# Optimization experiments

Measured on AMD Instinct MI355X. Metric: run time of the kernel, lower is better.

Reference implementation:

```python
import jax, jax.numpy as jnp
import numpy as np


def setup_inputs() -> dict:
    key = jax.random.key(0)
    k1, k2, k3, k4 = jax.random.split(key, 4)
    B, S, D = 2, 2048, 1024
    return {
        "X": jax.random.normal(k1, (B, S, D), dtype=jnp.float32),
        "W_q": jax.random.normal(k2, (D, D), dtype=jnp.float32),
        "W_k": jax.random.normal(k3, (D, D), dtype=jnp.float32),
        "W_v": jax.random.normal(k4, (D, D), dtype=jnp.float32),
        "n_heads": 16,
    }


def reference(X, W_q, W_k, W_v, n_heads):
    B, S, D = X.shape
    H = n_heads
    dh = D // H
    # QKV projections, split heads: [B,S,D] -> [H,B,S,dh]
    def split_heads(Y):
        return Y.reshape(B, S, H, dh).transpose(2, 0, 1, 3)
    Q = split_heads(X @ W_q)
    K = split_heads(X @ W_k)
    V = split_heads(X @ W_v)
    scale = 1.0 / jnp.sqrt(jnp.asarray(dh, dtype=X.dtype))
    # [H,B,S,S] attention scores (naive, matches the original)
    scores = jax.nn.softmax(jnp.einsum("hbqd,hbkd->hbqk", Q, K) * scale, axis=-1)
    out = jnp.einsum("hbqk,hbkd->hbqd", scores, V)  # [H,B,S,dh]
    # torch.concat(out, 0) over leading H dim -> [H*B, S, dh]
    return out.reshape(H * B, S, dh)
```

## Files before the change

kernel.cpp:

```cpp
#include <hip/hip_runtime.h>

typedef unsigned short u16;
typedef unsigned int u32;
typedef __bf16 bf16x8 __attribute__((ext_vector_type(8)));
typedef float f32x4 __attribute__((ext_vector_type(4)));
typedef float f32x16 __attribute__((ext_vector_type(16)));

#define WT_HI_E  ((size_t)0)
#define WT_LO_E  ((size_t)3 << 20)
#define X_HI_E   ((size_t)6 << 20)
#define X_LO_E   ((size_t)10 << 20)
#define Q_HI_E   ((size_t)14 << 20)
#define Q_LO_E   ((size_t)18 << 20)
#define K_HI_E   ((size_t)22 << 20)
#define K_LO_E   ((size_t)26 << 20)
#define V_HI_E   ((size_t)30 << 20)

__device__ __forceinline__ u16 bf16_rne(float x) {
  u32 u = __float_as_uint(x);
  u32 r = (u + 0x7fffu + ((u >> 16) & 1u)) >> 16;
  return (u16)r;
}
__device__ __forceinline__ float bf16_f(u16 h) {
  return __uint_as_float(((u32)h) << 16);
}

__device__ __forceinline__ void gload16(const u16* g, u16* l) {
  __builtin_amdgcn_global_load_lds(
      (const __attribute__((address_space(1))) void*)g,
      (__attribute__((address_space(3))) void*)l, 16, 0, 0);
}

__global__ __launch_bounds__(256) void k_xsplit(const float* __restrict__ X,
                                                u16* __restrict__ ws) {
  u16* xh = ws + X_HI_E;
  u16* xl = ws + X_LO_E;
  size_t i = ((size_t)blockIdx.x * 256 + threadIdx.x) * 8;
  float4 a = *(const float4*)(X + i);
  float4 b = *(const float4*)(X + i + 4);
  float v[8] = {a.x, a.y, a.z, a.w, b.x, b.y, b.z, b.w};
  u32 Hh[4], Ll[4];
#pragma unroll
  for (int j = 0; j < 4; j++) {
    u16 h0 = bf16_rne(v[2 * j]);
    u16 l0 = bf16_rne(v[2 * j] - bf16_f(h0));
    u16 h1 = bf16_rne(v[2 * j + 1]);
    u16 l1 = bf16_rne(v[2 * j + 1] - bf16_f(h1));
    Hh[j] = (u32)h0 | ((u32)h1 << 16);
    Ll[j] = (u32)l0 | ((u32)l1 << 16);
  }
  *(uint4*)(xh + i) = make_uint4(Hh[0], Hh[1], Hh[2], Hh[3]);
  *(uint4*)(xl + i) = make_uint4(Ll[0], Ll[1], Ll[2], Ll[3]);
}

__global__ __launch_bounds__(256) void k_wsplit(const float* __restrict__ w0,
                                                const float* __restrict__ w1,
                                                const float* __restrict__ w2,
                                                u16* __restrict__ ws) {
  int z = blockIdx.z;
  const float* W = (z == 0) ? w0 : ((z == 1) ? w1 : w2);
  u16* th = ws + WT_HI_E + (size_t)z * (1u << 20);
  u16* tl = ws + WT_LO_E + (size_t)z * (1u << 20);
  __shared__ float tile[32][33];
  int bx = blockIdx.x * 32, by = blockIdx.y * 32;
  int tx = threadIdx.x & 31, ty = threadIdx.x >> 5;
#pragma unroll
  for (int i = 0; i < 4; i++) {
    int r = ty + i * 8;
    tile[r][tx] = W[(size_t)(by + r) * 1024 + bx + tx];
  }
  __syncthreads();
#pragma unroll
  for (int i = 0; i < 4; i++) {
    int r = ty + i * 8;
    float v = tile[tx][r];
    int n = bx + r, k = by + tx;
    u16 h = bf16_rne(v);
    u16 l = bf16_rne(v - bf16_f(h));
    th[(size_t)n * 1024 + k] = h;
    tl[(size_t)n * 1024 + k] = l;
  }
}

__global__ __launch_bounds__(256) void k_proj(u16* __restrict__ ws) {
  int z = blockIdx.z;
  const u16* Xh = ws + X_HI_E;
  const u16* Xl = ws + X_LO_E;
  const u16* Wh = ws + WT_HI_E + (size_t)z * (1u << 20);
  const u16* Wl = ws + WT_LO_E + (size_t)z * (1u << 20);
  u16* dsth = ws + ((z == 0) ? Q_HI_E : ((z == 1) ? K_HI_E : V_HI_E));
  u16* dstl = (z == 0) ? (ws + Q_LO_E) : ((z == 1) ? (ws + K_LO_E) : (u16*)0);

  __shared__ u16 sXh[4096], sXl[4096], sWh[4096], sWl[4096];
  int M0 = blockIdx.y * 128, N0 = blockIdx.x * 128;
  int tid = threadIdx.x, lane = tid & 63, w = tid >> 6;
  int quad = lane >> 4, l16 = lane & 15;
  int mb = (w & 1) * 64, nb = (w >> 1) * 64;

  const f32x4 z4 = {0.f, 0.f, 0.f, 0.f};
  f32x4 acc[4][4];
#pragma unroll
  for (int i = 0; i < 4; i++)
#pragma unroll
    for (int j = 0; j < 4; j++) acc[i][j] = z4;

  for (int kk = 0; kk < 1024; kk += 32) {
    __syncthreads();
#pragma unroll
    for (int c2 = 0; c2 < 2; c2++) {
      int cb = c2 * 256 + w * 64;
      int c = cb + lane;
      int row = c >> 2, q8 = c & 3;
      size_t gx = (size_t)(M0 + row) * 1024 + kk + q8 * 8;
      size_t gw = (size_t)(N0 + row) * 1024 + kk + q8 * 8;
      gload16(Xh + gx, sXh + (size_t)cb * 8);
      gload16(Wh + gw, sWh + (size_t)cb * 8);
      if (z != 2) {
        gload16(Xl + gx, sXl + (size_t)cb * 8);
        gload16(Wl + gw, sWl + (size_t)cb * 8);
      }
    }
    __syncthreads();
    bf16x8 ah[4], bh[4];
#pragma unroll
    for (int i = 0; i < 4; i++) {
      ah[i] = *(const bf16x8*)&sXh[(mb + i * 16 + l16) * 32 + quad * 8];
      bh[i] = *(const bf16x8*)&sWh[(nb + i * 16 + l16) * 32 + quad * 8];
    }
    if (z != 2) {
      bf16x8 al[4], bl[4];
#pragma unroll
      for (int i = 0; i < 4; i++) {
        al[i] = *(const bf16x8*)&sXl[(mb + i * 16 + l16) * 32 + quad * 8];
        bl[i] = *(const bf16x8*)&sWl[(nb + i * 16 + l16) * 32 + quad * 8];
      }
#pragma unroll
      for (int i = 0; i < 4; i++)
#pragma unroll
        for (int j = 0; j < 4; j++) {
          f32x4 c0 = acc[i][j];
          c0 = __builtin_amdgcn_mfma_f32_16x16x32_bf16(ah[i], bh[j], c0, 0, 0, 0);
          c0 = __builtin_amdgcn_mfma_f32_16x16x32_bf16(ah[i], bl[j], c0, 0, 0, 0);
          c0 = __builtin_amdgcn_mfma_f32_16x16x32_bf16(al[i], bh[j], c0, 0, 0, 0);
          acc[i][j] = c0;
        }
    } else {
#pragma unroll
      for (int i = 0; i < 4; i++)
#pragma unroll
        for (int j = 0; j < 4; j++)
          acc[i][j] = __builtin_amdgcn_mfma_f32_16x16x32_bf16(ah[i], bh[j], acc[i][j], 0, 0, 0);
    }
  }

  if (z == 2) {
#pragma unroll
    for (int i = 0; i < 4; i++)
#pragma unroll
      for (int j = 0; j < 4; j++) {
        int mg = M0 + mb + i * 16 + quad * 4;
        int ng = N0 + nb + j * 16 + l16;
        int b = mg >> 11, s = mg & 2047;
        int hh = ng >> 6, d = ng & 63;
        int cp = ((s >> 3) & 7) ^ (d & 7);
        int ssw = (s & ~63) | (cp << 3) | (s & 7);
        u16 p0 = bf16_rne(acc[i][j][0]);
        u16 p1 = bf16_rne(acc[i][j][1]);
        u16 p2 = bf16_rne(acc[i][j][2]);
        u16 p3 = bf16_rne(acc[i][j][3]);
        *(uint2*)&dsth[((size_t)(hh * 2 + b) * 64 + d) * 2048 + ssw] =
            make_uint2((u32)p0 | ((u32)p1 << 16), (u32)p2 | ((u32)p3 << 16));
      }
  } else {
    float qscale = (z == 0) ? 0.125f : 1.0f;
#pragma unroll
    for (int i = 0; i < 4; i++)
#pragma unroll
      for (int j = 0; j < 4; j++)
#pragma unroll
        for (int r = 0; r < 4; r++) {
          int mg = M0 + mb + i * 16 + quad * 4 + r;
          int ng = N0 + nb + j * 16 + l16;
          int b = mg >> 11, s = mg & 2047;
          int hh = ng >> 6, d = ng & 63;
          int d2 = d;
          if (z == 1) d2 = ((((d >> 3) ^ (s & 7)) & 7) << 3) | (d & 7);
          size_t idx = ((size_t)(hh * 2 + b) * 2048 + s) * 64 + d2;
          float y = acc[i][j][r] * qscale;
          u16 h = bf16_rne(y);
          dsth[idx] = h;
          dstl[idx] = bf16_rne(y - bf16_f(h));
        }
  }
}

__global__ __launch_bounds__(256, 2) void k_attn(u16* __restrict__ ws,
                                                 float* __restrict__ out) {
  const u16* Qh = ws + Q_HI_E;
  const u16* Ql = ws + Q_LO_E;
  const u16* Kh = ws + K_HI_E;
  const u16* Kl = ws + K_LO_E;
  const u16* Vt = ws + V_HI_E;

  __shared__ u16 sKh[2][64][64], sKl[2][64][64], sVt[2][64][64];

  int id = blockIdx.x;
  int hb = id & 31, qb = id >> 5;
  int tid = threadIdx.x, w = tid >> 6, lane = tid & 63;
  int l31 = lane & 31, h = lane >> 5;
  size_t base = (size_t)hb * (2048 * 64);
  int qw0 = qb * 128 + w * 32;

  int srow = lane >> 3, sch = lane & 7;

  auto stage = [&](int buf, int kt) {
#pragma unroll
    for (int b2 = 0; b2 < 2; b2++) {
      int rr = w * 16 + b2 * 8;
      size_t kg = base + (size_t)(kt + rr + srow) * 64 + sch * 8;
      gload16(Kh + kg, &sKh[buf][rr][0]);
      gload16(Kl + kg, &sKl[buf][rr][0]);
      size_t vg = base + (size_t)(rr + srow) * 2048 + kt + sch * 8;
      gload16(Vt + vg, &sVt[buf][rr][0]);
    }
  };

  stage(0, 0);

  bf16x8 qh[4], ql[4];
#pragma unroll
  for (int ks = 0; ks < 4; ks++) {
    size_t off = base + (size_t)(qw0 + l31) * 64 + ks * 16 + h * 8;
    qh[ks] = *(const bf16x8*)(Qh + off);
    ql[ks] = *(const bf16x8*)(Ql + off);
  }

  f32x16 o[2];
#pragma unroll
  for (int i = 0; i < 16; i++) { o[0][i] = 0.f; o[1][i] = 0.f; }
  float mr = -1e30f, lr = 0.f;

  auto rdA = [&](const u16 t[64][64], int mt, int ks) -> bf16x8 {
    int ch = ((ks * 2 + h) ^ (l31 & 7)) * 8;
    return *(const bf16x8*)&t[mt * 32 + l31][ch];
  };

  for (int it = 0; it < 32; it++) {
    __syncthreads();
    if (it + 1 < 32) stage((it + 1) & 1, (it + 1) * 64);
    int buf = it & 1;

    f32x16 sc[2];
#pragma unroll
    for (int i = 0; i < 16; i++) { sc[0][i] = 0.f; sc[1][i] = 0.f; }
#pragma unroll
    for (int ks = 0; ks < 4; ks++)
#pragma unroll
      for (int mt = 0; mt < 2; mt++) {
        bf16x8 kh = rdA(sKh[buf], mt, ks);
        bf16x8 kl = rdA(sKl[buf], mt, ks);
        sc[mt] = __builtin_amdgcn_mfma_f32_32x32x16_bf16(kh, qh[ks], sc[mt], 0, 0, 0);
        sc[mt] = __builtin_amdgcn_mfma_f32_32x32x16_bf16(kh, ql[ks], sc[mt], 0, 0, 0);
        sc[mt] = __builtin_amdgcn_mfma_f32_32x32x16_bf16(kl, qh[ks], sc[mt], 0, 0, 0);
      }

    float mx = sc[0][0];
#pragma unroll
    for (int i = 0; i < 16; i++) {
      mx = fmaxf(mx, sc[0][i]);
      mx = fmaxf(mx, sc[1][i]);
    }
    mx = fmaxf(mx, __shfl_xor(mx, 32));
    float mnew = fmaxf(mr, mx);
    float alpha = __expf(mr - mnew);
    mr = mnew;
    float rs = 0.f;
    u32 pk[2][8];
#pragma unroll
    for (int t = 0; t < 2; t++)
#pragma unroll
      for (int i = 0; i < 8; i++) {
        float p0 = __expf(sc[t][2 * i] - mnew);
        float p1 = __expf(sc[t][2 * i + 1] - mnew);
        rs += p0 + p1;
        u32 a = __float_as_uint(p0) + 0x8000u;
        u32 b = __float_as_uint(p1) + 0x8000u;
        pk[t][i] = __builtin_amdgcn_perm(b, a, 0x07060302u);
      }
    rs += __shfl_xor(rs, 32);
    lr = lr * alpha + rs;
#pragma unroll
    for (int i = 0; i < 16; i++) {
      o[0][i] *= alpha;
      o[1][i] *= alpha;
    }

#pragma unroll
    for (int ks = 0; ks < 4; ks++) {
      int t = ks >> 1, c = ks & 1;
      u32 b0 = pk[t][c * 4 + 0], b1 = pk[t][c * 4 + 1];
      u32 b2 = pk[t][c * 4 + 2], b3 = pk[t][c * 4 + 3];
      u32 rA = (u32)__shfl_xor((int)(h ? b0 : b2), 32);
      u32 rB = (u32)__shfl_xor((int)(h ? b1 : b3), 32);
      uint4 fb = h ? make_uint4(rA, rB, b2, b3) : make_uint4(b0, b1, rA, rB);
      bf16x8 pfrag = *(bf16x8*)&fb;
#pragma unroll
      for (int mt = 0; mt < 2; mt++) {
        bf16x8 vb = rdA(sVt[buf], mt, ks);
        o[mt] = __builtin_amdgcn_mfma_f32_32x32x16_bf16(vb, pfrag, o[mt], 0, 0, 0);
      }
    }
  }

  float inv = 1.f / lr;
  size_t grow = (size_t)hb * 2048 + qw0 + l31;
#pragma unroll
  for (int mt = 0; mt < 2; mt++)
#pragma unroll
    for (int g2 = 0; g2 < 4; g2++) {
      int d0 = mt * 32 + g2 * 8 + 4 * h;
      float4 v = make_float4(o[mt][g2 * 4 + 0] * inv, o[mt][g2 * 4 + 1] * inv,
                             o[mt][g2 * 4 + 2] * inv, o[mt][g2 * 4 + 3] * inv);
      *(float4*)(out + grow * 64 + d0) = v;
    }
}

extern "C" void kernel_launch(void* const* d_in, const int* in_sizes, int n_in,
                              void* d_out, int out_size, void* d_ws, size_t ws_size,
                              hipStream_t stream) {
  const float* X = (const float*)d_in[0];
  const float* Wq = (const float*)d_in[1];
  const float* Wk = (const float*)d_in[2];
  const float* Wv = (const float*)d_in[3];
  u16* ws = (u16*)d_ws;
  float* out = (float*)d_out;

  k_xsplit<<<dim3(2048), dim3(256), 0, stream>>>(X, ws);
  k_wsplit<<<dim3(32, 32, 3), dim3(256), 0, stream>>>(Wq, Wk, Wv, ws);
  k_proj<<<dim3(8, 32, 3), dim3(256), 0, stream>>>(ws);
  k_attn<<<dim3(512), dim3(256), 0, stream>>>(ws, out);
}
```

Measured before the change: 243.3 us.

## Split attention over two key halves with combine kernel, exp2 softmax, higher occupancy

Splits the key dimension of the attention kernel into two halves, doubling the grid to 1024 blocks. Each half writes unnormalized partial outputs plus its running max and sum, and a new combine kernel merges them. The Q scale now folds in log2(e) so softmax can use native exp2. Shared memory drops from double to single buffering (with an extra barrier) so occupancy can rise to 4 blocks per CU. The cost is extra global traffic and one more launch for the combine step, and loads are no longer overlapped with compute inside a block.

```diff
diff --git a/kernel.cpp b/kernel.cpp
--- a/kernel.cpp
+++ b/kernel.cpp
@@ -5,6 +5,8 @@
 typedef __bf16 bf16x8 __attribute__((ext_vector_type(8)));
 typedef float f32x4 __attribute__((ext_vector_type(4)));
 typedef float f32x16 __attribute__((ext_vector_type(16)));
+
+extern "C" __device__ float __ocml_native_exp2_f32(float);
 
 #define WT_HI_E  ((size_t)0)
 #define WT_LO_E  ((size_t)3 << 20)
@@ -15,6 +17,8 @@
 #define K_HI_E   ((size_t)22 << 20)
 #define K_LO_E   ((size_t)26 << 20)
 #define V_HI_E   ((size_t)30 << 20)
+#define O1_E     ((size_t)0)
+#define ML_E     ((size_t)9 << 20)
 
 __device__ __forceinline__ u16 bf16_rne(float x) {
   u32 u = __float_as_uint(x);
@@ -172,7 +176,7 @@
             make_uint2((u32)p0 | ((u32)p1 << 16), (u32)p2 | ((u32)p3 << 16));
       }
   } else {
-    float qscale = (z == 0) ? 0.125f : 1.0f;
+    float qscale = (z == 0) ? (0.125f * 1.4426950408889634f) : 1.0f;
 #pragma unroll
     for (int i = 0; i < 4; i++)
 #pragma unroll
@@ -194,18 +198,24 @@
   }
 }
 
-__global__ __launch_bounds__(256, 2) void k_attn(u16* __restrict__ ws,
+__global__ __launch_bounds__(256, 4) void k_attn(u16* __restrict__ ws,
                                                  float* __restrict__ out) {
   const u16* Qh = ws + Q_HI_E;
   const u16* Ql = ws + Q_LO_E;
   const u16* Kh = ws + K_HI_E;
   const u16* Kl = ws + K_LO_E;
   const u16* Vt = ws + V_HI_E;
-
-  __shared__ u16 sKh[2][64][64], sKl[2][64][64], sVt[2][64][64];
+  float* o1 = (float*)(ws + O1_E);
+  float* ml = (float*)(ws + ML_E);
+
+  __shared__ u16 sKh[64][64], sKl[64][64], sVt[64][64];
 
   int id = blockIdx.x;
-  int hb = id & 31, qb = id >> 5;
+  int hb = id & 31;
+  int rem = id >> 5;
+  int qb = rem >> 1, split = rem & 1;
+  int kt0 = split * 1024;
+
   int tid = threadIdx.x, w = tid >> 6, lane = tid & 63;
   int l31 = lane & 31, h = lane >> 5;
   size_t base = (size_t)hb * (2048 * 64);
@@ -213,20 +223,6 @@
 
   int srow = lane >> 3, sch = lane & 7;
 
-  auto stage = [&](int buf, int kt) {
-#pragma unroll
-    for (int b2 = 0; b2 < 2; b2++) {
-      int rr = w * 16 + b2 * 8;
-      size_t kg = base + (size_t)(kt + rr + srow) * 64 + sch * 8;
-      gload16(Kh + kg, &sKh[buf][rr][0]);
-      gload16(Kl + kg, &sKl[buf][rr][0]);
-      size_t vg = base + (size_t)(rr + srow) * 2048 + kt + sch * 8;
-      gload16(Vt + vg, &sVt[buf][rr][0]);
-    }
-  };
-
-  stage(0, 0);
-
   bf16x8 qh[4], ql[4];
 #pragma unroll
   for (int ks = 0; ks < 4; ks++) {
@@ -245,10 +241,19 @@
     return *(const bf16x8*)&t[mt * 32 + l31][ch];
   };
 
-  for (int it = 0; it < 32; it++) {
+  for (int it = 0; it < 16; it++) {
+    int kt = kt0 + it * 64;
     __syncthreads();
-    if (it + 1 < 32) stage((it + 1) & 1, (it + 1) * 64);
-    int buf = it & 1;
+#pragma unroll
+    for (int b2 = 0; b2 < 2; b2++) {
+      int rr = w * 16 + b2 * 8;
+      size_t kg = base + (size_t)(kt + rr + srow) * 64 + sch * 8;
+      gload16(Kh + kg, &sKh[rr][0]);
+      gload16(Kl + kg, &sKl[rr][0]);
+      size_t vg = base + (size_t)(rr + srow) * 2048 + kt + sch * 8;
+      gload16(Vt + vg, &sVt[rr][0]);
+    }
+    __syncthreads();
 
     f32x16 sc[2];
 #pragma unroll
@@ -257,8 +262,8 @@
     for (int ks = 0; ks < 4; ks++)
 #pragma unroll
       for (int mt = 0; mt < 2; mt++) {
-        bf16x8 kh = rdA(sKh[buf], mt, ks);
-        bf16x8 kl = rdA(sKl[buf], mt, ks);
+        bf16x8 kh = rdA(sKh, mt, ks);
+        bf16x8 kl = rdA(sKl, mt, ks);
         sc[mt] = __builtin_amdgcn_mfma_f32_32x32x16_bf16(kh, qh[ks], sc[mt], 0, 0, 0);
         sc[mt] = __builtin_amdgcn_mfma_f32_32x32x16_bf16(kh, ql[ks], sc[mt], 0, 0, 0);
         sc[mt] = __builtin_amdgcn_mfma_f32_32x32x16_bf16(kl, qh[ks], sc[mt], 0, 0, 0);
@@ -272,7 +277,7 @@
     }
     mx = fmaxf(mx, __shfl_xor(mx, 32));
     float mnew = fmaxf(mr, mx);
-    float alpha = __expf(mr - mnew);
+    float alpha = __ocml_native_exp2_f32(mr - mnew);
     mr = mnew;
     float rs = 0.f;
     u32 pk[2][8];
@@ -280,8 +285,8 @@
     for (int t = 0; t < 2; t++)
 #pragma unroll
       for (int i = 0; i < 8; i++) {
-        float p0 = __expf(sc[t][2 * i] - mnew);
-        float p1 = __expf(sc[t][2 * i + 1] - mnew);
+        float p0 = __ocml_native_exp2_f32(sc[t][2 * i] - mnew);
+        float p1 = __ocml_native_exp2_f32(sc[t][2 * i + 1] - mnew);
         rs += p0 + p1;
         u32 a = __float_as_uint(p0) + 0x8000u;
         u32 b = __float_as_uint(p1) + 0x8000u;
@@ -306,23 +311,49 @@
       bf16x8 pfrag = *(bf16x8*)&fb;
 #pragma unroll
       for (int mt = 0; mt < 2; mt++) {
-        bf16x8 vb = rdA(sVt[buf], mt, ks);
+        bf16x8 vb = rdA(sVt, mt, ks);
         o[mt] = __builtin_amdgcn_mfma_f32_32x32x16_bf16(vb, pfrag, o[mt], 0, 0, 0);
       }
     }
   }
 
-  float inv = 1.f / lr;
-  size_t grow = (size_t)hb * 2048 + qw0 + l31;
+  float* op = split ? o1 : out;
+  float* mlp = ml + (size_t)split * 131072;
+  size_t g = (size_t)hb * 2048 + qw0 + l31;
+  if (h == 0) {
+    mlp[g] = mr;
+    mlp[65536 + g] = lr;
+  }
 #pragma unroll
   for (int mt = 0; mt < 2; mt++)
 #pragma unroll
     for (int g2 = 0; g2 < 4; g2++) {
       int d0 = mt * 32 + g2 * 8 + 4 * h;
-      float4 v = make_float4(o[mt][g2 * 4 + 0] * inv, o[mt][g2 * 4 + 1] * inv,
-                             o[mt][g2 * 4 + 2] * inv, o[mt][g2 * 4 + 3] * inv);
-      *(float4*)(out + grow * 64 + d0) = v;
-    }
+      float4 v = make_float4(o[mt][g2 * 4 + 0], o[mt][g2 * 4 + 1],
+                             o[mt][g2 * 4 + 2], o[mt][g2 * 4 + 3]);
+      *(float4*)(op + g * 64 + d0) = v;
+    }
+}
+
+__global__ __launch_bounds__(256) void k_combine(const u16* __restrict__ ws,
+                                                 float* __restrict__ out) {
+  const float* o1 = (const float*)(ws + O1_E);
+  const float* ml = (const float*)(ws + ML_E);
+  size_t idx = (size_t)blockIdx.x * 256 + threadIdx.x;
+  size_t g = idx >> 4;
+  float m0 = ml[g], l0 = ml[65536 + g];
+  float m1 = ml[131072 + g], l1 = ml[196608 + g];
+  float M = fmaxf(m0, m1);
+  float w0 = __ocml_native_exp2_f32(m0 - M), w1 = __ocml_native_exp2_f32(m1 - M);
+  float inv = 1.f / (l0 * w0 + l1 * w1);
+  float4 a = ((const float4*)out)[idx];
+  float4 b = ((const float4*)o1)[idx];
+  float4 r;
+  r.x = (a.x * w0 + b.x * w1) * inv;
+  r.y = (a.y * w0 + b.y * w1) * inv;
+  r.z = (a.z * w0 + b.z * w1) * inv;
+  r.w = (a.w * w0 + b.w * w1) * inv;
+  ((float4*)out)[idx] = r;
 }
 
 extern "C" void kernel_launch(void* const* d_in, const int* in_sizes, int n_in,
@@ -338,5 +369,6 @@
   k_xsplit<<<dim3(2048), dim3(256), 0, stream>>>(X, ws);
   k_wsplit<<<dim3(32, 32, 3), dim3(256), 0, stream>>>(Wq, Wk, Wv, ws);
   k_proj<<<dim3(8, 32, 3), dim3(256), 0, stream>>>(ws);
-  k_attn<<<dim3(512), dim3(256), 0, stream>>>(ws, out);
-}
+  k_attn<<<dim3(1024), dim3(256), 0, stream>>>(ws, out);
+  k_combine<<<dim3(4096), dim3(256), 0, stream>>>(ws, out);
+}
```

New measurement: 255.9 us. 1.05x slower.
